# Kernel tuning notes

Hardware: AMD Instinct MI355X
Metric: run time of the kernel (lower is better)

## Reference

```python
import jax, jax.numpy as jnp
import numpy as np

B, W, H, C = 4, 32, 32, 128   # image feature map
S, D = 256, 512               # text seq len, text embed dim
NC = 64                       # num_channels (attention inner dim)


def setup_inputs() -> dict:
    key = jax.random.key(0)
    ks = jax.random.split(key, 16)
    def dense(k, din, dout):
        return jax.random.normal(k, (din, dout), jnp.float32) / np.sqrt(din)
    return {
        "x": jax.random.normal(ks[0], (B, W, H, C), jnp.float32),
        "s": jax.random.normal(ks[1], (B, S, D), jnp.float32),
        "a": jax.random.randint(ks[2], (B, S), 0, 2).astype(jnp.float32),
        "Wq": dense(ks[3], C, NC),  "bq": jnp.zeros((NC,), jnp.float32),
        "Wkx": dense(ks[4], C, NC), "bkx": jnp.zeros((NC,), jnp.float32),
        "Wvx": dense(ks[5], C, NC), "bvx": jnp.zeros((NC,), jnp.float32),
        "Wks": dense(ks[6], D, NC), "bks": jnp.zeros((NC,), jnp.float32),
        "Wvs": dense(ks[7], D, NC), "bvs": jnp.zeros((NC,), jnp.float32),
        "Wout": dense(ks[8], NC, C), "bout": jnp.zeros((C,), jnp.float32),
        "ln_scale": jnp.ones((C,), jnp.float32),
        "ln_bias": jnp.zeros((C,), jnp.float32),
    }


def reference(x, s, a, Wq, bq, Wkx, bkx, Wvx, bvx, Wks, bks, Wvs, bvs,
              Wout, bout, ln_scale, ln_bias):
    nc = Wq.shape[-1]
    # mask text embeddings: repeat(a,'b s -> b s d') * s
    te = s * a[:, :, None]
    # projections
    q = x @ Wq + bq            # (b,w,h,c)
    kx = x @ Wkx + bkx         # (b,w,h,c)
    vx = x @ Vx_dummy if False else x @ Wvx + bvx
    ks = te @ Wks + bks        # (b,s,c)
    vs = te @ Wvs + bvs        # (b,s,c)
    # broadcast-add spatial and text keys/values -> (b,w,h,s,c)
    k = kx[:, :, :, None, :] + ks[:, None, None, :, :]
    v = vx[:, :, :, None, :] + vs[:, None, None, :, :]
    # attention matrix over channels: v^T @ k contracted over s -> (b,w,h,c,c)
    attn = jnp.einsum('bwhsc,bwhsd->bwhcd', v, k) / jnp.sqrt(jnp.asarray(nc, x.dtype))
    attn = jax.nn.softmax(attn, axis=-1)
    # q applied through the channel-channel attention -> (b,w,h,c)
    out = jnp.einsum('bwhj,bwhjk->bwhk', q, attn)
    # output projection back to x channels, residual, layernorm
    out = out @ Wout + bout
    x = x + out
    mu = jnp.mean(x, axis=-1, keepdims=True)
    var = jnp.var(x, axis=-1, keepdims=True)
    x = (x - mu) * jax.lax.rsqrt(var + 1e-6) * ln_scale + ln_bias
    return x
```

## Files before the change

### kernel.cpp

```cpp
#include <hip/hip_runtime.h>
#include <hip/hip_bf16.h>

#define BB 4
#define SS 256
#define DD 512
#define CC 128
#define NC 64
#define PXB 4

__global__ __launch_bounds__(192) void xproj_kernel(
    const float* __restrict__ x,
    const float* __restrict__ Wq,  const float* __restrict__ bq,
    const float* __restrict__ Wkx, const float* __restrict__ bkx,
    const float* __restrict__ Wvx, const float* __restrict__ bvx,
    float* __restrict__ P)
{
    __shared__ float xl[8][CC];
    const int t = threadIdx.x;
    const int w = t >> 6, lane = t & 63;
    const int px0 = blockIdx.x * 8;

    {
        const float4* x4 = (const float4*)(x + (size_t)px0 * CC);
        for (int i = t; i < 8 * CC / 4; i += 192)
            ((float4*)&xl[0][0])[i] = x4[i];
    }
    __syncthreads();

    const float* __restrict__ Wm = (w == 0) ? Wq : (w == 1 ? Wkx : Wvx);
    const float* __restrict__ bm = (w == 0) ? bq : (w == 1 ? bkx : bvx);
    float a0=0.f,a1=0.f,a2=0.f,a3=0.f,a4=0.f,a5=0.f,a6=0.f,a7=0.f;
    #pragma unroll 4
    for (int k = 0; k < CC; ++k) {
        const float wv = Wm[(size_t)k * NC + lane];
        a0 = fmaf(xl[0][k], wv, a0);
        a1 = fmaf(xl[1][k], wv, a1);
        a2 = fmaf(xl[2][k], wv, a2);
        a3 = fmaf(xl[3][k], wv, a3);
        a4 = fmaf(xl[4][k], wv, a4);
        a5 = fmaf(xl[5][k], wv, a5);
        a6 = fmaf(xl[6][k], wv, a6);
        a7 = fmaf(xl[7][k], wv, a7);
    }
    const float bb = bm[lane];
    float* dst = P + (size_t)px0 * 192 + w * 64 + lane;
    dst[0*192] = a0 + bb; dst[1*192] = a1 + bb;
    dst[2*192] = a2 + bb; dst[3*192] = a3 + bb;
    dst[4*192] = a4 + bb; dst[5*192] = a5 + bb;
    dst[6*192] = a6 + bb; dst[7*192] = a7 + bb;
}

__global__ __launch_bounds__(256) void text_proj_kernel(
    const float* __restrict__ s, const float* __restrict__ a,
    const float* __restrict__ Wks, const float* __restrict__ bks,
    const float* __restrict__ Wvs, const float* __restrict__ bvs,
    float* __restrict__ ksw, float* __restrict__ vsw)
{
    __shared__ float tel[2][DD];
    __shared__ float part[2][2][2][NC];
    const int t = threadIdx.x;
    const int w = t >> 6, lane = t & 63;
    const int row0 = blockIdx.x * 2;

    {
        const float4* s4 = (const float4*)(s + (size_t)row0 * DD);
        const int i = t;
        const int r = i >> 7;
        const float am = a[row0 + r];
        float4 v = s4[i];
        v.x *= am; v.y *= am; v.z *= am; v.w *= am;
        ((float4*)&tel[0][0])[i] = v;
    }
    __syncthreads();

    const int m = w & 1, h = w >> 1;
    const int kb = h * 256;
    const int cg = (lane & 15) * 4;
    const int ksub = lane >> 4;
    const float* __restrict__ Wm = m ? Wvs : Wks;

    float4 acc0 = {0,0,0,0}, acc1 = {0,0,0,0};
    #pragma unroll 4
    for (int j = 0; j < 64; ++j) {
        const int k = kb + 4 * j + ksub;
        const float4 wv = *(const float4*)(Wm + (size_t)k * NC + cg);
        const float t0 = tel[0][k];
        const float t1 = tel[1][k];
        acc0.x = fmaf(t0, wv.x, acc0.x); acc0.y = fmaf(t0, wv.y, acc0.y);
        acc0.z = fmaf(t0, wv.z, acc0.z); acc0.w = fmaf(t0, wv.w, acc0.w);
        acc1.x = fmaf(t1, wv.x, acc1.x); acc1.y = fmaf(t1, wv.y, acc1.y);
        acc1.z = fmaf(t1, wv.z, acc1.z); acc1.w = fmaf(t1, wv.w, acc1.w);
    }
    #pragma unroll
    for (int off = 16; off <= 32; off <<= 1) {
        acc0.x += __shfl_down(acc0.x, off); acc0.y += __shfl_down(acc0.y, off);
        acc0.z += __shfl_down(acc0.z, off); acc0.w += __shfl_down(acc0.w, off);
        acc1.x += __shfl_down(acc1.x, off); acc1.y += __shfl_down(acc1.y, off);
        acc1.z += __shfl_down(acc1.z, off); acc1.w += __shfl_down(acc1.w, off);
    }
    if (lane < 16) {
        *(float4*)&part[m][h][0][cg] = acc0;
        *(float4*)&part[m][h][1][cg] = acc1;
    }
    __syncthreads();

    {
        const int mm = t >> 7, r = (t >> 6) & 1, col = t & 63;
        const float v = part[mm][0][r][col] + part[mm][1][r][col]
                      + (mm ? bvs[col] : bks[col]);
        float* dst = mm ? vsw : ksw;
        dst[(size_t)(row0 + r) * NC + col] = v;
    }
}

__global__ __launch_bounds__(256) void reduce_kernel(
    const float* __restrict__ ksw, const float* __restrict__ vsw,
    float* __restrict__ Mw, float* __restrict__ Ksw, float* __restrict__ Vsw)
{
    __shared__ float pm[4][NC], pk[4][NC], pv[4];
    const int t = threadIdx.x, w = t >> 6, d = t & 63;
    const int b = blockIdx.x >> 6, c = blockIdx.x & 63;
    const float* __restrict__ vsb = vsw + (size_t)b * SS * NC;
    const float* __restrict__ ksb = ksw + (size_t)b * SS * NC;
    float acc = 0.f, ks_ = 0.f, vs_ = 0.f;
    #pragma unroll 4
    for (int j = 0; j < 64; ++j) {
        const int s2 = w * 64 + j;
        const float vv = vsb[s2 * NC + c];
        const float kv = ksb[s2 * NC + d];
        acc = fmaf(vv, kv, acc);
        ks_ += kv; vs_ += vv;
    }
    pm[w][d] = acc; pk[w][d] = ks_;
    if (d == 0) pv[w] = vs_;
    __syncthreads();
    if (t < 64) {
        Mw[((size_t)b * NC + c) * NC + t] = pm[0][t] + pm[1][t] + pm[2][t] + pm[3][t];
        if (c == 0) Ksw[b * NC + t] = pk[0][t] + pk[1][t] + pk[2][t] + pk[3][t];
        if (t == 0) Vsw[b * NC + c] = pv[0] + pv[1] + pv[2] + pv[3];
    }
}

__global__ __launch_bounds__(256) void pixel_kernel(
    const float* __restrict__ x, const float* __restrict__ P,
    const float* __restrict__ Wout, const float* __restrict__ bout,
    const float* __restrict__ ln_scale, const float* __restrict__ ln_bias,
    const float* __restrict__ Mw, const float* __restrict__ Ksw,
    const float* __restrict__ Vsw,
    float* __restrict__ out)
{
    __shared__ float Ml[NC * 65];
    __shared__ float projl[PXB][192];
    __shared__ float xl[PXB][CC];
    __shared__ float rsl[PXB][NC];
    __shared__ float mxl[PXB][NC];
    __shared__ float outl[PXB][NC];
    __shared__ float Ksl[NC], Vsl[NC];
    __shared__ float redl[2][2][4];

    const int t = threadIdx.x;
    const int w = t >> 6, lane = t & 63;
    const int px0g = blockIdx.x * PXB;
    const int b = px0g >> 10;

    {
        const float4* P4 = (const float4*)(P + (size_t)px0g * 192);
        for (int i = t; i < PXB * 192 / 4; i += 256)
            ((float4*)&projl[0][0])[i] = P4[i];
        const float4* x4 = (const float4*)(x + (size_t)px0g * CC);
        for (int i = t; i < PXB * CC / 4; i += 256)
            ((float4*)&xl[0][0])[i] = x4[i];
        const float* Mb = Mw + (size_t)b * NC * NC;
        for (int i = t; i < NC * NC; i += 256)
            Ml[(i >> 6) * 65 + (i & 63)] = Mb[i];
        if (t < NC) { Ksl[t] = Ksw[b * NC + t]; Vsl[t] = Vsw[b * NC + t]; }
    }
    __syncthreads();

    {
        const int px = w, c = lane;
        const float vxc = projl[px][128 + c];
        const float qc  = projl[px][c];
        const float uc  = fmaf(256.0f, vxc, Vsl[c]);
        float row[NC];
        float mx = -3.4e38f;
        #pragma unroll
        for (int d = 0; d < NC; ++d) {
            const float A = fmaf(uc, projl[px][64 + d],
                                 fmaf(vxc, Ksl[d], Ml[c * 65 + d])) * 0.125f;
            row[d] = A;
            mx = fmaxf(mx, A);
        }
        float sum = 0.f;
        #pragma unroll
        for (int d = 0; d < NC; ++d) sum += __expf(row[d] - mx);
        rsl[px][c] = qc / sum;
        mxl[px][c] = mx;
    }
    __syncthreads();

    {
        const int px = w, d = lane;
        const float kxd = projl[px][64 + d];
        const float Ksd = Ksl[d];
        float acc = 0.f;
        #pragma unroll 4
        for (int c = 0; c < NC; ++c) {
            const float vxc = projl[px][128 + c];
            const float uc = fmaf(256.0f, vxc, Vsl[c]);
            const float A = fmaf(uc, kxd, fmaf(vxc, Ksd, Ml[c * 65 + d])) * 0.125f;
            acc = fmaf(rsl[px][c], __expf(A - mxl[px][c]), acc);
        }
        outl[px][d] = acc;
    }
    __syncthreads();

    {
        const int col = t & 127;
        const int pxg = t >> 7;
        const int px0 = 2 * pxg, px1 = px0 + 1;
        float acc0 = 0.f, acc1 = 0.f;
        #pragma unroll 4
        for (int k = 0; k < NC; ++k) {
            const float wv = Wout[k * CC + col];
            acc0 = fmaf(outl[px0][k], wv, acc0);
            acc1 = fmaf(outl[px1][k], wv, acc1);
        }
        const float bb = bout[col];
        const float y0 = acc0 + bb + xl[px0][col];
        const float y1 = acc1 + bb + xl[px1][col];

        float s10 = y0, s20 = y0 * y0, s11 = y1, s21 = y1 * y1;
        #pragma unroll
        for (int off = 32; off >= 1; off >>= 1) {
            s10 += __shfl_down(s10, off);
            s20 += __shfl_down(s20, off);
            s11 += __shfl_down(s11, off);
            s21 += __shfl_down(s21, off);
        }
        const int half = (t >> 6) & 1;
        if (lane == 0) {
            redl[pxg][half][0] = s10; redl[pxg][half][1] = s20;
            redl[pxg][half][2] = s11; redl[pxg][half][3] = s21;
        }
        __syncthreads();
        const float S10 = redl[pxg][0][0] + redl[pxg][1][0];
        const float S20 = redl[pxg][0][1] + redl[pxg][1][1];
        const float S11 = redl[pxg][0][2] + redl[pxg][1][2];
        const float S21 = redl[pxg][0][3] + redl[pxg][1][3];
        const float mu0 = S10 * (1.f / 128.f);
        const float var0 = S20 * (1.f / 128.f) - mu0 * mu0;
        const float mu1 = S11 * (1.f / 128.f);
        const float var1 = S21 * (1.f / 128.f) - mu1 * mu1;
        const float r0 = rsqrtf(var0 + 1e-6f), r1 = rsqrtf(var1 + 1e-6f);
        const float gg = ln_scale[col], be = ln_bias[col];
        out[(size_t)(px0g + px0) * CC + col] = (y0 - mu0) * r0 * gg + be;
        out[(size_t)(px0g + px1) * CC + col] = (y1 - mu1) * r1 * gg + be;
    }
}

extern "C" void kernel_launch(void* const* d_in, const int* in_sizes, int n_in,
                              void* d_out, int out_size, void* d_ws, size_t ws_size,
                              hipStream_t stream) {
    const float* x        = (const float*)d_in[0];
    const float* s        = (const float*)d_in[1];
    const float* a        = (const float*)d_in[2];
    const float* Wq       = (const float*)d_in[3];
    const float* bq       = (const float*)d_in[4];
    const float* Wkx      = (const float*)d_in[5];
    const float* bkx      = (const float*)d_in[6];
    const float* Wvx      = (const float*)d_in[7];
    const float* bvx      = (const float*)d_in[8];
    const float* Wks      = (const float*)d_in[9];
    const float* bks      = (const float*)d_in[10];
    const float* Wvs      = (const float*)d_in[11];
    const float* bvs      = (const float*)d_in[12];
    const float* Wout     = (const float*)d_in[13];
    const float* bout     = (const float*)d_in[14];
    const float* ln_scale = (const float*)d_in[15];
    const float* ln_bias  = (const float*)d_in[16];

    float* ws  = (float*)d_ws;
    float* ksw = ws;
    float* vsw = ws + 65536;
    float* Mw  = ws + 131072;
    float* Ksw = ws + 147456;
    float* Vsw = ws + 147712;
    float* Pw  = ws + 147968;

    xproj_kernel<<<512, 192, 0, stream>>>(x, Wq, bq, Wkx, bkx, Wvx, bvx, Pw);
    text_proj_kernel<<<(BB * SS) / 2, 256, 0, stream>>>(s, a, Wks, bks, Wvs, bvs, ksw, vsw);
    reduce_kernel<<<BB * NC, 256, 0, stream>>>(ksw, vsw, Mw, Ksw, Vsw);
    pixel_kernel<<<(BB * 1024) / PXB, 256, 0, stream>>>(
        x, Pw, Wout, bout, ln_scale, ln_bias, Mw, Ksw, Vsw, (float*)d_out);
}
```

Baseline: 127.6 us.

## Fuse pixel and text projection kernels into one launch; recompute softmax logits

Merges the pixel q/kx/vx projection kernel and the text key/value projection kernel into a single launch that branches on block index. This removes one kernel launch and lets the two independent projections run concurrently. The pixel projection now uses float4 weight loads with a k-split across lanes followed by a shuffle reduction. The pixel kernel also stops storing the 64-entry logit row in registers and recomputes the logits in the exp-sum pass, trading extra FMAs for lower register pressure.

Measured after the change: 118.2 us. 7.4% less time.

```diff
diff --git a/kernel.cpp b/kernel.cpp
--- a/kernel.cpp
+++ b/kernel.cpp
@@ -8,108 +8,120 @@
 #define NC 64
 #define PXB 4
 
-__global__ __launch_bounds__(192) void xproj_kernel(
+__global__ __launch_bounds__(256) void fused_proj_kernel(
     const float* __restrict__ x,
     const float* __restrict__ Wq,  const float* __restrict__ bq,
     const float* __restrict__ Wkx, const float* __restrict__ bkx,
     const float* __restrict__ Wvx, const float* __restrict__ bvx,
-    float* __restrict__ P)
-{
-    __shared__ float xl[8][CC];
-    const int t = threadIdx.x;
-    const int w = t >> 6, lane = t & 63;
-    const int px0 = blockIdx.x * 8;
-
-    {
-        const float4* x4 = (const float4*)(x + (size_t)px0 * CC);
-        for (int i = t; i < 8 * CC / 4; i += 192)
-            ((float4*)&xl[0][0])[i] = x4[i];
-    }
-    __syncthreads();
-
-    const float* __restrict__ Wm = (w == 0) ? Wq : (w == 1 ? Wkx : Wvx);
-    const float* __restrict__ bm = (w == 0) ? bq : (w == 1 ? bkx : bvx);
-    float a0=0.f,a1=0.f,a2=0.f,a3=0.f,a4=0.f,a5=0.f,a6=0.f,a7=0.f;
-    #pragma unroll 4
-    for (int k = 0; k < CC; ++k) {
-        const float wv = Wm[(size_t)k * NC + lane];
-        a0 = fmaf(xl[0][k], wv, a0);
-        a1 = fmaf(xl[1][k], wv, a1);
-        a2 = fmaf(xl[2][k], wv, a2);
-        a3 = fmaf(xl[3][k], wv, a3);
-        a4 = fmaf(xl[4][k], wv, a4);
-        a5 = fmaf(xl[5][k], wv, a5);
-        a6 = fmaf(xl[6][k], wv, a6);
-        a7 = fmaf(xl[7][k], wv, a7);
-    }
-    const float bb = bm[lane];
-    float* dst = P + (size_t)px0 * 192 + w * 64 + lane;
-    dst[0*192] = a0 + bb; dst[1*192] = a1 + bb;
-    dst[2*192] = a2 + bb; dst[3*192] = a3 + bb;
-    dst[4*192] = a4 + bb; dst[5*192] = a5 + bb;
-    dst[6*192] = a6 + bb; dst[7*192] = a7 + bb;
-}
-
-__global__ __launch_bounds__(256) void text_proj_kernel(
     const float* __restrict__ s, const float* __restrict__ a,
     const float* __restrict__ Wks, const float* __restrict__ bks,
     const float* __restrict__ Wvs, const float* __restrict__ bvs,
-    float* __restrict__ ksw, float* __restrict__ vsw)
+    float* __restrict__ P, float* __restrict__ ksw, float* __restrict__ vsw)
 {
     __shared__ float tel[2][DD];
     __shared__ float part[2][2][2][NC];
+    __shared__ float xl[8][CC];
+
     const int t = threadIdx.x;
     const int w = t >> 6, lane = t & 63;
-    const int row0 = blockIdx.x * 2;
-
-    {
-        const float4* s4 = (const float4*)(s + (size_t)row0 * DD);
-        const int i = t;
-        const int r = i >> 7;
-        const float am = a[row0 + r];
-        float4 v = s4[i];
-        v.x *= am; v.y *= am; v.z *= am; v.w *= am;
-        ((float4*)&tel[0][0])[i] = v;
-    }
-    __syncthreads();
-
-    const int m = w & 1, h = w >> 1;
-    const int kb = h * 256;
-    const int cg = (lane & 15) * 4;
-    const int ksub = lane >> 4;
-    const float* __restrict__ Wm = m ? Wvs : Wks;
-
-    float4 acc0 = {0,0,0,0}, acc1 = {0,0,0,0};
-    #pragma unroll 4
-    for (int j = 0; j < 64; ++j) {
-        const int k = kb + 4 * j + ksub;
-        const float4 wv = *(const float4*)(Wm + (size_t)k * NC + cg);
-        const float t0 = tel[0][k];
-        const float t1 = tel[1][k];
-        acc0.x = fmaf(t0, wv.x, acc0.x); acc0.y = fmaf(t0, wv.y, acc0.y);
-        acc0.z = fmaf(t0, wv.z, acc0.z); acc0.w = fmaf(t0, wv.w, acc0.w);
-        acc1.x = fmaf(t1, wv.x, acc1.x); acc1.y = fmaf(t1, wv.y, acc1.y);
-        acc1.z = fmaf(t1, wv.z, acc1.z); acc1.w = fmaf(t1, wv.w, acc1.w);
-    }
-    #pragma unroll
-    for (int off = 16; off <= 32; off <<= 1) {
-        acc0.x += __shfl_down(acc0.x, off); acc0.y += __shfl_down(acc0.y, off);
-        acc0.z += __shfl_down(acc0.z, off); acc0.w += __shfl_down(acc0.w, off);
-        acc1.x += __shfl_down(acc1.x, off); acc1.y += __shfl_down(acc1.y, off);
-        acc1.z += __shfl_down(acc1.z, off); acc1.w += __shfl_down(acc1.w, off);
-    }
-    if (lane < 16) {
-        *(float4*)&part[m][h][0][cg] = acc0;
-        *(float4*)&part[m][h][1][cg] = acc1;
-    }
-    __syncthreads();
-
-    {
-        const int mm = t >> 7, r = (t >> 6) & 1, col = t & 63;
-        const float v = part[mm][0][r][col] + part[mm][1][r][col]
-                      + (mm ? bvs[col] : bks[col]);
-        float* dst = mm ? vsw : ksw;
-        dst[(size_t)(row0 + r) * NC + col] = v;
+
+    if (blockIdx.x < 512) {
+        const int px0 = blockIdx.x * 8;
+        {
+            const float4* x4 = (const float4*)(x + (size_t)px0 * CC);
+            ((float4*)&xl[0][0])[t] = x4[t];
+        }
+        __syncthreads();
+        if (w < 3) {
+            const float* __restrict__ Wm = (w == 0) ? Wq : (w == 1 ? Wkx : Wvx);
+            const float* __restrict__ bm = (w == 0) ? bq : (w == 1 ? bkx : bvx);
+            const int ksub = lane >> 4;
+            const int cg = (lane & 15) * 4;
+            float4 acc[8] = {};
+            #pragma unroll 4
+            for (int j = 0; j < 32; ++j) {
+                const int k = 4 * j + ksub;
+                const float4 wv = *(const float4*)(Wm + (size_t)k * NC + cg);
+                #pragma unroll
+                for (int px = 0; px < 8; ++px) {
+                    const float xv = xl[px][k];
+                    acc[px].x = fmaf(xv, wv.x, acc[px].x);
+                    acc[px].y = fmaf(xv, wv.y, acc[px].y);
+                    acc[px].z = fmaf(xv, wv.z, acc[px].z);
+                    acc[px].w = fmaf(xv, wv.w, acc[px].w);
+                }
+            }
+            #pragma unroll
+            for (int px = 0; px < 8; ++px) {
+                #pragma unroll
+                for (int off = 16; off <= 32; off <<= 1) {
+                    acc[px].x += __shfl_down(acc[px].x, off);
+                    acc[px].y += __shfl_down(acc[px].y, off);
+                    acc[px].z += __shfl_down(acc[px].z, off);
+                    acc[px].w += __shfl_down(acc[px].w, off);
+                }
+            }
+            if (ksub == 0) {
+                const float4 bb = *(const float4*)(bm + cg);
+                #pragma unroll
+                for (int px = 0; px < 8; ++px) {
+                    float4 v;
+                    v.x = acc[px].x + bb.x; v.y = acc[px].y + bb.y;
+                    v.z = acc[px].z + bb.z; v.w = acc[px].w + bb.w;
+                    *(float4*)(P + (size_t)(px0 + px) * 192 + w * 64 + cg) = v;
+                }
+            }
+        }
+    } else {
+        const int row0 = (blockIdx.x - 512) * 2;
+        {
+            const float4* s4 = (const float4*)(s + (size_t)row0 * DD);
+            const int r = t >> 7;
+            const float am = a[row0 + r];
+            float4 v = s4[t];
+            v.x *= am; v.y *= am; v.z *= am; v.w *= am;
+            ((float4*)&tel[0][0])[t] = v;
+        }
+        __syncthreads();
+
+        const int m = w & 1, h = w >> 1;
+        const int kb = h * 256;
+        const int cg = (lane & 15) * 4;
+        const int ksub = lane >> 4;
+        const float* __restrict__ Wm = m ? Wvs : Wks;
+
+        float4 acc0 = {0,0,0,0}, acc1 = {0,0,0,0};
+        #pragma unroll 4
+        for (int j = 0; j < 64; ++j) {
+            const int k = kb + 4 * j + ksub;
+            const float4 wv = *(const float4*)(Wm + (size_t)k * NC + cg);
+            const float t0 = tel[0][k];
+            const float t1 = tel[1][k];
+            acc0.x = fmaf(t0, wv.x, acc0.x); acc0.y = fmaf(t0, wv.y, acc0.y);
+            acc0.z = fmaf(t0, wv.z, acc0.z); acc0.w = fmaf(t0, wv.w, acc0.w);
+            acc1.x = fmaf(t1, wv.x, acc1.x); acc1.y = fmaf(t1, wv.y, acc1.y);
+            acc1.z = fmaf(t1, wv.z, acc1.z); acc1.w = fmaf(t1, wv.w, acc1.w);
+        }
+        #pragma unroll
+        for (int off = 16; off <= 32; off <<= 1) {
+            acc0.x += __shfl_down(acc0.x, off); acc0.y += __shfl_down(acc0.y, off);
+            acc0.z += __shfl_down(acc0.z, off); acc0.w += __shfl_down(acc0.w, off);
+            acc1.x += __shfl_down(acc1.x, off); acc1.y += __shfl_down(acc1.y, off);
+            acc1.z += __shfl_down(acc1.z, off); acc1.w += __shfl_down(acc1.w, off);
+        }
+        if (lane < 16) {
+            *(float4*)&part[m][h][0][cg] = acc0;
+            *(float4*)&part[m][h][1][cg] = acc1;
+        }
+        __syncthreads();
+
+        {
+            const int mm = t >> 7, r = (t >> 6) & 1, col = t & 63;
+            const float v = part[mm][0][r][col] + part[mm][1][r][col]
+                          + (mm ? bvs[col] : bks[col]);
+            float* dst = mm ? vsw : ksw;
+            dst[(size_t)(row0 + r) * NC + col] = v;
+        }
     }
 }
 
@@ -182,18 +194,20 @@
         const float vxc = projl[px][128 + c];
         const float qc  = projl[px][c];
         const float uc  = fmaf(256.0f, vxc, Vsl[c]);
-        float row[NC];
         float mx = -3.4e38f;
         #pragma unroll
         for (int d = 0; d < NC; ++d) {
             const float A = fmaf(uc, projl[px][64 + d],
                                  fmaf(vxc, Ksl[d], Ml[c * 65 + d])) * 0.125f;
-            row[d] = A;
             mx = fmaxf(mx, A);
         }
         float sum = 0.f;
         #pragma unroll
-        for (int d = 0; d < NC; ++d) sum += __expf(row[d] - mx);
+        for (int d = 0; d < NC; ++d) {
+            const float A = fmaf(uc, projl[px][64 + d],
+                                 fmaf(vxc, Ksl[d], Ml[c * 65 + d])) * 0.125f;
+            sum += __expf(A - mx);
+        }
         rsl[px][c] = qc / sum;
         mxl[px][c] = mx;
     }
@@ -288,8 +302,8 @@
     float* Vsw = ws + 147712;
     float* Pw  = ws + 147968;
 
-    xproj_kernel<<<512, 192, 0, stream>>>(x, Wq, bq, Wkx, bkx, Wvx, bvx, Pw);
-    text_proj_kernel<<<(BB * SS) / 2, 256, 0, stream>>>(s, a, Wks, bks, Wvs, bvs, ksw, vsw);
+    fused_proj_kernel<<<1024, 256, 0, stream>>>(
+        x, Wq, bq, Wkx, bkx, Wvx, bvx, s, a, Wks, bks, Wvs, bvs, Pw, ksw, vsw);
     reduce_kernel<<<BB * NC, 256, 0, stream>>>(ksw, vsw, Mw, Ksw, Vsw);
     pixel_kernel<<<(BB * 1024) / PXB, 256, 0, stream>>>(
         x, Pw, Wout, bout, ln_scale, ln_bias, Mw, Ksw, Vsw, (float*)d_out);
```
